# Kernel tuning notes

Measured on AMD Instinct MI355X. Metric: run time of the kernel, lower is better.

## Reference

```python
import jax, jax.numpy as jnp
import numpy as np

B, N, X, Y, W1, W2 = 2, 6, 8, 8, 8, 8
DIM, HEADS, DHEAD = 128, 4, 32
HD = HEADS * DHEAD
EPS = 1e-5


def setup_inputs() -> dict:
    key = jax.random.key(0)
    ks = jax.random.split(key, 12)
    d = {}
    d['q'] = jax.random.normal(ks[0], (B, N, X, Y, W1, W2, DIM), jnp.float32)
    d['k'] = jax.random.normal(ks[1], (B, N, X, Y, W1, W2, DIM), jnp.float32)
    d['v'] = jax.random.normal(ks[2], (B, N, X, Y, W1, W2, DIM), jnp.float32)
    d['skip'] = jax.random.normal(ks[3], (B, X, Y, W1, W2, DIM), jnp.float32)
    d['head_gate'] = jax.random.uniform(ks[4], (HEADS,), jnp.float32, 0.5, 1.5)
    # LayerNorm affine params (slightly perturbed so grads are nontrivial)
    d['ln_q_w'] = 1.0 + 0.1 * jax.random.normal(ks[5], (DIM,), jnp.float32)
    d['ln_q_b'] = jnp.zeros((DIM,), jnp.float32)
    d['ln_k_w'] = 1.0 + 0.1 * jax.random.normal(ks[6], (DIM,), jnp.float32)
    d['ln_k_b'] = jnp.zeros((DIM,), jnp.float32)
    d['ln_v_w'] = 1.0 + 0.1 * jax.random.normal(ks[7], (DIM,), jnp.float32)
    d['ln_v_b'] = jnp.zeros((DIM,), jnp.float32)
    # Linear weights, stored as (in, out) so x @ w + b
    s = 0.02
    d['wq'] = s * jax.random.normal(ks[8], (DIM, HD), jnp.float32)
    d['bq'] = jnp.zeros((HD,), jnp.float32)
    d['wk'] = s * jax.random.normal(ks[9], (DIM, HD), jnp.float32)
    d['bk'] = jnp.zeros((HD,), jnp.float32)
    d['wv'] = s * jax.random.normal(ks[10], (DIM, HD), jnp.float32)
    d['bv'] = jnp.zeros((HD,), jnp.float32)
    d['wp'] = s * jax.random.normal(ks[11], (HD, DIM), jnp.float32)
    d['bp'] = jnp.zeros((DIM,), jnp.float32)
    return d


def _ln(x, w, b):
    mu = jnp.mean(x, axis=-1, keepdims=True)
    var = jnp.mean(jnp.square(x - mu), axis=-1, keepdims=True)
    return (x - mu) * jax.lax.rsqrt(var + EPS) * w + b


def _windows(t):
    # (b, n, x, y, w1, w2, d) -> (b, x*y, n*w1*w2, d)
    b, n, x, y, w1, w2, dd = t.shape
    return t.transpose(0, 2, 3, 1, 4, 5, 6).reshape(b, x * y, n * w1 * w2, dd)


def _heads(t):
    # (b, l, t, HEADS*DHEAD) -> (b, m, l, t, DHEAD)
    b, l, tt, _ = t.shape
    return t.reshape(b, l, tt, HEADS, DHEAD).transpose(0, 3, 1, 2, 4)


def reference(q, k, v, skip, head_gate,
              ln_q_w, ln_q_b, ln_k_w, ln_k_b, ln_v_w, ln_v_b,
              wq, bq, wk, bk, wv, bv, wp, bp):
    b, n, x, y, w1, w2, _ = q.shape
    scale = DHEAD ** -0.5
    qh = _heads(_ln(_windows(q), ln_q_w, ln_q_b) @ wq + bq) * scale
    kh = _heads(_ln(_windows(k), ln_k_w, ln_k_b) @ wk + bk)
    vh = _heads(_ln(_windows(v), ln_v_w, ln_v_b) @ wv + bv)
    # per-window attention: l = x*y windows, Q = K = n*w1*w2 tokens
    dot = jnp.einsum('bmlqd,bmlkd->bmlqk', qh, kh)
    dot = dot * head_gate[None, :, None, None, None]
    att = jax.nn.softmax(dot, axis=-1)
    a = jnp.einsum('bmlqk,bmlkd->bmlqd', att, vh)
    a = a.transpose(0, 2, 3, 1, 4).reshape(b, x * y, n * w1 * w2, HD)
    out = a.reshape(b, x, y, n, w1, w2, HD).transpose(0, 3, 1, 2, 4, 5, 6)
    z = out @ wp + bp          # (b, n, x, y, w1, w2, dim)
    z = jnp.mean(z, axis=1)    # mean over agents n
    return z + skip
```

## Files before the change

kernel.cpp:

```cpp
#include <hip/hip_runtime.h>
#include <hip/hip_bf16.h>
#include <cstddef>

#define NB     2
#define NA     6
#define NWIN   64
#define NTOK   384
#define DIM    128
#define NHEADS 4
#define DHEAD  32

typedef __attribute__((ext_vector_type(8))) short short8;
typedef __attribute__((ext_vector_type(4))) float f32x4;

__device__ __forceinline__ unsigned short f2bf(float f) {
    __hip_bfloat16 h = __float2bfloat16(f);
    return *reinterpret_cast<unsigned short*>(&h);
}
__device__ __forceinline__ float bf2f(unsigned short u) {
    union { unsigned int i; float f; } x; x.i = ((unsigned int)u) << 16; return x.f;
}

#define QSCALE (0.17677669529663687f * 1.4426950408889634f)

__global__ __launch_bounds__(256) void wprep_kernel(
    const float* __restrict__ wq, const float* __restrict__ wk,
    const float* __restrict__ wv,
    const float* __restrict__ lnqw, const float* __restrict__ lnkw,
    const float* __restrict__ lnvw,
    const float* __restrict__ lnqb, const float* __restrict__ lnkb,
    const float* __restrict__ lnvb,
    const float* __restrict__ bq, const float* __restrict__ bk,
    const float* __restrict__ bv, const float* __restrict__ gate,
    unsigned short* __restrict__ wt,
    float* __restrict__ scol, float* __restrict__ tcol)
{
    const int bid = blockIdx.x;
    if (bid < 192) {
        const int e = bid * 256 + threadIdx.x;
        const int mat = e >> 14, i = e & 16383;
        const int kk = i >> 7, c = i & 127;
        const float* src = (mat == 0) ? wq : (mat == 1) ? wk : wv;
        const float* lnw = (mat == 0) ? lnqw : (mat == 1) ? lnkw : lnvw;
        const float s = (mat == 0) ? (QSCALE * gate[c >> 5]) : 1.0f;
        wt[(mat << 14) + c * DIM + kk] = f2bf(src[i] * lnw[kk] * s);
        return;
    }
    const int mat = bid - 192;
    const int c = threadIdx.x;
    if (c >= DIM) return;
    const float* src  = (mat == 0) ? wq : (mat == 1) ? wk : wv;
    const float* lnw  = (mat == 0) ? lnqw : (mat == 1) ? lnkw : lnvw;
    const float* lnb  = (mat == 0) ? lnqb : (mat == 1) ? lnkb : lnvb;
    const float* bias = (mat == 0) ? bq : (mat == 1) ? bk : bv;
    float sa[8] = {0.f,0.f,0.f,0.f,0.f,0.f,0.f,0.f};
    float ta[8] = {0.f,0.f,0.f,0.f,0.f,0.f,0.f,0.f};
#pragma unroll
    for (int k0 = 0; k0 < DIM; k0 += 8) {
        float w0 = src[(k0+0)*DIM+c], w1 = src[(k0+1)*DIM+c];
        float w2 = src[(k0+2)*DIM+c], w3 = src[(k0+3)*DIM+c];
        float w4 = src[(k0+4)*DIM+c], w5 = src[(k0+5)*DIM+c];
        float w6 = src[(k0+6)*DIM+c], w7 = src[(k0+7)*DIM+c];
        sa[0] += lnw[k0+0]*w0; ta[0] += lnb[k0+0]*w0;
        sa[1] += lnw[k0+1]*w1; ta[1] += lnb[k0+1]*w1;
        sa[2] += lnw[k0+2]*w2; ta[2] += lnb[k0+2]*w2;
        sa[3] += lnw[k0+3]*w3; ta[3] += lnb[k0+3]*w3;
        sa[4] += lnw[k0+4]*w4; ta[4] += lnb[k0+4]*w4;
        sa[5] += lnw[k0+5]*w5; ta[5] += lnb[k0+5]*w5;
        sa[6] += lnw[k0+6]*w6; ta[6] += lnb[k0+6]*w6;
        sa[7] += lnw[k0+7]*w7; ta[7] += lnb[k0+7]*w7;
    }
    const float s = ((sa[0]+sa[1])+(sa[2]+sa[3]))+((sa[4]+sa[5])+(sa[6]+sa[7]));
    const float t = ((ta[0]+ta[1])+(ta[2]+ta[3]))+((ta[4]+ta[5])+(ta[6]+ta[7]));
    const float qs = (mat == 0) ? (QSCALE * gate[c >> 5]) : 1.0f;
    scol[mat * DIM + c] = s * qs;
    tcol[mat * DIM + c] = (t + bias[c]) * qs;
}

#define ACC8(p, q) do { \
    s  += ((p.x + p.y) + (p.z + p.w)) + ((q.x + q.y) + (q.z + q.w)); \
    s2 += ((p.x*p.x + p.y*p.y) + (p.z*p.z + p.w*p.w)) \
        + ((q.x*q.x + q.y*q.y) + (q.z*q.z + q.w*q.w)); } while (0)
#define CVT8(p, q) ({ short8 o_; \
    o_[0]=(short)f2bf(p.x); o_[1]=(short)f2bf(p.y); o_[2]=(short)f2bf(p.z); o_[3]=(short)f2bf(p.w); \
    o_[4]=(short)f2bf(q.x); o_[5]=(short)f2bf(q.y); o_[6]=(short)f2bf(q.z); o_[7]=(short)f2bf(q.w); o_; })

__global__ __launch_bounds__(384) void proj_kernel(
    const float* __restrict__ qx, const float* __restrict__ kx,
    const float* __restrict__ vx,
    const unsigned short* __restrict__ wt,
    const float* __restrict__ scol, const float* __restrict__ tcol,
    unsigned short* __restrict__ qh, unsigned short* __restrict__ kh,
    unsigned short* __restrict__ vh)
{
    __shared__ unsigned short Wl[DIM * DIM];

    const int bid  = blockIdx.x;
    const int mode = bid >> 8;
    const int rr   = bid & 255;
    const int b = rr >> 7, l = (rr >> 1) & 63, ng = rr & 1;

    const float* xin = (mode == 0) ? qx : (mode == 1) ? kx : vx;
    const unsigned short* wtm = wt + (mode << 14);
    const float* sc = scol + mode * DIM;
    const float* tc = tcol + mode * DIM;
    unsigned short* outp = (mode == 0) ? qh : (mode == 1) ? kh : vh;

    const int wv_ = threadIdx.x / 64;
    const int lane = threadIdx.x & 63;
    const int g = lane >> 4, qc = lane & 15;
    const int n  = ng * 3 + (wv_ >> 1);
    const int t0 = (wv_ & 1) * 32;

    short8 wbuf0 = {0,0,0,0,0,0,0,0}, wbuf1 = wbuf0, wbuf2 = wbuf0,
           wbuf3 = wbuf0, wbuf4 = wbuf0, wbuf5 = wbuf0;
    {
        const int e0 = threadIdx.x;
        wbuf0 = *(const short8*)&wtm[(e0 +    0) * 8];
        wbuf1 = *(const short8*)&wtm[(e0 +  384) * 8];
        wbuf2 = *(const short8*)&wtm[(e0 +  768) * 8];
        wbuf3 = *(const short8*)&wtm[(e0 + 1152) * 8];
        wbuf4 = *(const short8*)&wtm[(e0 + 1536) * 8];
        if (e0 + 1920 < 2048) wbuf5 = *(const short8*)&wtm[(e0 + 1920) * 8];
    }

    const float* xp0 = xin + ((size_t)((b * NA + n) * NWIN + l) * 64 + t0 + qc) * DIM + 8 * g;
    const float* xp1 = xp0 + 16 * DIM;
    const float4 u0 = *(const float4*)(xp0 + 0);
    const float4 u1 = *(const float4*)(xp0 + 4);
    const float4 u2 = *(const float4*)(xp0 + 32);
    const float4 u3 = *(const float4*)(xp0 + 36);
    const float4 u4 = *(const float4*)(xp0 + 64);
    const float4 u5 = *(const float4*)(xp0 + 68);
    const float4 u6 = *(const float4*)(xp0 + 96);
    const float4 u7 = *(const float4*)(xp0 + 100);
    const float4 y0 = *(const float4*)(xp1 + 0);
    const float4 y1 = *(const float4*)(xp1 + 4);
    const float4 y2 = *(const float4*)(xp1 + 32);
    const float4 y3 = *(const float4*)(xp1 + 36);
    const float4 y4 = *(const float4*)(xp1 + 64);
    const float4 y5 = *(const float4*)(xp1 + 68);
    const float4 y6 = *(const float4*)(xp1 + 96);
    const float4 y7 = *(const float4*)(xp1 + 100);

    {
        const int e0 = threadIdx.x;
#define WSTORE(eo, bufv) do { const int e_ = e0 + eo; \
        const int col_ = e_ >> 4, k8_ = (e_ & 15) * 8; \
        *(short8*)&Wl[col_ * DIM + (k8_ ^ ((col_ & 7) << 3))] = bufv; } while (0)
        WSTORE(0, wbuf0); WSTORE(384, wbuf1); WSTORE(768, wbuf2);
        WSTORE(1152, wbuf3); WSTORE(1536, wbuf4);
        if (e0 + 1920 < 2048) WSTORE(1920, wbuf5);
#undef WSTORE
    }

    float mu0, rs0, mu1, rs1;
    {
        float s = 0.f, s2 = 0.f;
        ACC8(u0, u1); ACC8(u2, u3); ACC8(u4, u5); ACC8(u6, u7);
        s  += __shfl_xor(s, 16);  s  += __shfl_xor(s, 32);
        s2 += __shfl_xor(s2, 16); s2 += __shfl_xor(s2, 32);
        mu0 = s * (1.0f / 128.0f);
        rs0 = rsqrtf(s2 * (1.0f / 128.0f) - mu0 * mu0 + 1e-5f);
    }
    {
        float s = 0.f, s2 = 0.f;
        ACC8(y0, y1); ACC8(y2, y3); ACC8(y4, y5); ACC8(y6, y7);
        s  += __shfl_xor(s, 16);  s  += __shfl_xor(s, 32);
        s2 += __shfl_xor(s2, 16); s2 += __shfl_xor(s2, 32);
        mu1 = s * (1.0f / 128.0f);
        rs1 = rsqrtf(s2 * (1.0f / 128.0f) - mu1 * mu1 + 1e-5f);
    }

    short8 af0[4], af1[4];
    af0[0] = CVT8(u0, u1); af0[1] = CVT8(u2, u3);
    af0[2] = CVT8(u4, u5); af0[3] = CVT8(u6, u7);
    af1[0] = CVT8(y0, y1); af1[1] = CVT8(y2, y3);
    af1[2] = CVT8(y4, y5); af1[3] = CVT8(y6, y7);
    __syncthreads();

    float m0[4], r0[4], m1[4], r1[4];
    if (mode == 2) {
#pragma unroll
        for (int r = 0; r < 4; ++r) {
            m0[r] = __shfl(mu0, 4 * g + r); r0[r] = __shfl(rs0, 4 * g + r);
            m1[r] = __shfl(mu1, 4 * g + r); r1[r] = __shfl(rs1, 4 * g + r);
        }
    }

    const f32x4 z = {0.f, 0.f, 0.f, 0.f};
    const int swz = (qc & 7) << 3;

#pragma unroll
    for (int ct = 0; ct < 8; ++ct) {
        const int col = ct * 16 + qc;
        short8 wf[4];
#pragma unroll
        for (int c = 0; c < 4; ++c)
            wf[c] = *(const short8*)&Wl[col * DIM + ((c * 32 + 8 * g) ^ swz)];

        f32x4 a0 = z, a1 = z;
        if (mode == 2) {
#pragma unroll
            for (int c = 0; c < 4; ++c) {
                a0 = __builtin_amdgcn_mfma_f32_16x16x32_bf16(af0[c], wf[c], a0, 0, 0, 0);
                a1 = __builtin_amdgcn_mfma_f32_16x16x32_bf16(af1[c], wf[c], a1, 0, 0, 0);
            }
            const float s_c = sc[col], t_c = tc[col];
            const int head = ct >> 1;
            const int d = (ct & 1) * 16 + qc;
            const size_t rowb = ((size_t)(b * NHEADS + head) * NWIN + l) * DHEAD + d;
            unsigned short* dst = outp + rowb * NTOK + n * 64 + t0 + 4 * g;
            ushort4 o;
            o.x = f2bf(r0[0] * (a0[0] - m0[0] * s_c) + t_c);
            o.y = f2bf(r0[1] * (a0[1] - m0[1] * s_c) + t_c);
            o.z = f2bf(r0[2] * (a0[2] - m0[2] * s_c) + t_c);
            o.w = f2bf(r0[3] * (a0[3] - m0[3] * s_c) + t_c);
            *(ushort4*)&dst[0] = o;
            o.x = f2bf(r1[0] * (a1[0] - m1[0] * s_c) + t_c);
            o.y = f2bf(r1[1] * (a1[1] - m1[1] * s_c) + t_c);
            o.z = f2bf(r1[2] * (a1[2] - m1[2] * s_c) + t_c);
            o.w = f2bf(r1[3] * (a1[3] - m1[3] * s_c) + t_c);
            *(ushort4*)&dst[16] = o;
        } else {
#pragma unroll
            for (int c = 0; c < 4; ++c) {
                a0 = __builtin_amdgcn_mfma_f32_16x16x32_bf16(wf[c], af0[c], a0, 0, 0, 0);
                a1 = __builtin_amdgcn_mfma_f32_16x16x32_bf16(wf[c], af1[c], a1, 0, 0, 0);
            }
            const int head = ct >> 1;
            const int d0 = (ct & 1) * 16 + 4 * g;
            const float4 s4 = *(const float4*)&sc[ct * 16 + 4 * g];
            const float4 t4 = *(const float4*)&tc[ct * 16 + 4 * g];
            const size_t hb = (size_t)(b * NHEADS + head) * NWIN + l;
            unsigned short* dst = outp + (hb * NTOK + n * 64 + t0 + qc) * DHEAD + d0;
            ushort4 o;
            o.x = f2bf(rs0 * (a0[0] - mu0 * s4.x) + t4.x);
            o.y = f2bf(rs0 * (a0[1] - mu0 * s4.y) + t4.y);
            o.z = f2bf(rs0 * (a0[2] - mu0 * s4.z) + t4.z);
            o.w = f2bf(rs0 * (a0[3] - mu0 * s4.w) + t4.w);
            *(ushort4*)&dst[0] = o;
            o.x = f2bf(rs1 * (a1[0] - mu1 * s4.x) + t4.x);
            o.y = f2bf(rs1 * (a1[1] - mu1 * s4.y) + t4.y);
            o.z = f2bf(rs1 * (a1[2] - mu1 * s4.z) + t4.z);
            o.w = f2bf(rs1 * (a1[3] - mu1 * s4.w) + t4.w);
            *(ushort4*)&dst[16 * DHEAD] = o;
        }
    }
}

__global__ __launch_bounds__(256) void attn_kernel(
    const unsigned short* __restrict__ qh, const unsigned short* __restrict__ kh,
    const unsigned short* __restrict__ vt, unsigned short* __restrict__ aout)
{
    __shared__ unsigned short P[4][3][16][40];

    const int tid  = threadIdx.x;
    const int w    = tid >> 6;
    const int lane = tid & 63;
    const int g    = lane >> 4;
    const int qc   = lane & 15;

    const int raw = blockIdx.x;
    const int p    = (raw >> 4) * 8 + (raw & 7);
    const int half = (raw >> 3) & 1;
    const int b = p >> 8, h = (p >> 6) & 3, l = p & 63;
    const size_t base = (size_t)((b * NHEADS + h) * NWIN + l) * (NTOK * DHEAD);
    const unsigned short* Qp = qh + base;
    const unsigned short* Kp = kh + base;
    const unsigned short* Vp = vt + base;

    short8 qf[3];
#pragma unroll
    for (int j = 0; j < 3; ++j)
        qf[j] = *(const short8*)(Qp + (size_t)(((half * 4 + w) * 3 + j) * 16 + qc) * DHEAD + 8 * g);

    f32x4 o0[3], o1[3];
    float psum[3];
    const f32x4 z = {0.f, 0.f, 0.f, 0.f};
#pragma unroll
    for (int j = 0; j < 3; ++j) { o0[j] = z; o1[j] = z; psum[j] = 0.f; }

    for (int kc = 0; kc < 12; ++kc) {
        const int k0 = kc * 32;
        const short8 ka0 = *(const short8*)(Kp + (size_t)(k0 + qc) * DHEAD + 8 * g);
        const short8 ka1 = *(const short8*)(Kp + (size_t)(k0 + 16 + qc) * DHEAD + 8 * g);
        const short8 vb0 = *(const short8*)(Vp + (size_t)qc * NTOK + k0 + 8 * g);
        const short8 vb1 = *(const short8*)(Vp + (size_t)(16 + qc) * NTOK + k0 + 8 * g);

#pragma unroll
        for (int j = 0; j < 3; ++j) {
            f32x4 s0 = __builtin_amdgcn_mfma_f32_16x16x32_bf16(ka0, qf[j], z, 0, 0, 0);
            f32x4 s1 = __builtin_amdgcn_mfma_f32_16x16x32_bf16(ka1, qf[j], z, 0, 0, 0);
            const float e0 = exp2f(s0[0]), e1 = exp2f(s0[1]), e2 = exp2f(s0[2]), e3 = exp2f(s0[3]);
            const float e4 = exp2f(s1[0]), e5 = exp2f(s1[1]), e6 = exp2f(s1[2]), e7 = exp2f(s1[3]);
            psum[j] += ((e0 + e1) + (e2 + e3)) + ((e4 + e5) + (e6 + e7));
            ushort4 pw0, pw1;
            pw0.x = f2bf(e0); pw0.y = f2bf(e1); pw0.z = f2bf(e2); pw0.w = f2bf(e3);
            pw1.x = f2bf(e4); pw1.y = f2bf(e5); pw1.z = f2bf(e6); pw1.w = f2bf(e7);
            *(ushort4*)&P[w][j][qc][4 * g]      = pw0;
            *(ushort4*)&P[w][j][qc][16 + 4 * g] = pw1;
        }
#pragma unroll
        for (int j = 0; j < 3; ++j) {
            const short8 pa = *(const short8*)&P[w][j][qc][8 * g];
            o0[j] = __builtin_amdgcn_mfma_f32_16x16x32_bf16(pa, vb0, o0[j], 0, 0, 0);
            o1[j] = __builtin_amdgcn_mfma_f32_16x16x32_bf16(pa, vb1, o1[j], 0, 0, 0);
        }
    }

#pragma unroll
    for (int j = 0; j < 3; ++j) {
        float ps = psum[j];
        ps += __shfl_xor(ps, 16);
        ps += __shfl_xor(ps, 32);
        const float inv = 1.0f / ps;
        const int q0 = ((half * 4 + w) * 3 + j) * 16;
        const size_t ob = ((size_t)(b * NWIN + l) * NTOK + q0) * (NHEADS * DHEAD) + h * DHEAD + qc;
#pragma unroll
        for (int r = 0; r < 4; ++r) {
            const float iv = __shfl(inv, 4 * g + r);
            aout[ob + (size_t)(4 * g + r) * (NHEADS * DHEAD)]      = f2bf(o0[j][r] * iv);
            aout[ob + (size_t)(4 * g + r) * (NHEADS * DHEAD) + 16] = f2bf(o1[j][r] * iv);
        }
    }
}

__global__ __launch_bounds__(256) void outproj_kernel(
    const unsigned short* __restrict__ a, const float* __restrict__ wp,
    const float* __restrict__ bp, const float* __restrict__ skip,
    float* __restrict__ outp)
{
    __shared__ float at[DIM * 68];
    __shared__ float wl[DIM * 64];

    const int tid = threadIdx.x;
    const int bid = blockIdx.x;
    const int b = bid >> 7, l = (bid >> 1) & 63, cg = bid & 1;
    const int c0 = cg * 64;

#pragma unroll
    for (int rep = 0; rep < 8; ++rep) {
        const int idx = rep * 256 + tid;
        const int row = idx >> 4, cc4 = idx & 15;
        *(float4*)&wl[row * 64 + cc4 * 4] = *(const float4*)&wp[row * 128 + c0 + cc4 * 4];
    }

    const size_t abase = (size_t)(b * NWIN + l) * NTOK * DIM;
#pragma unroll
    for (int r = 0; r < 32; ++r) {
        const int f = tid + 256 * r;
        const int w_ = f >> 7, d = f & 127;
        float s = 0.f;
#pragma unroll
        for (int n = 0; n < NA; ++n)
            s += bf2f(a[abase + (size_t)(n * 64 + w_) * DIM + d]);
        at[d * 68 + w_] = s * (1.0f / 6.0f);
    }
    __syncthreads();

    const int cx = tid & 15, ty = tid >> 4;
    float acc[4][4];
#pragma unroll
    for (int i = 0; i < 4; ++i)
#pragma unroll
        for (int j = 0; j < 4; ++j) acc[i][j] = 0.f;

#pragma unroll 4
    for (int i = 0; i < DIM; ++i) {
        const float4 wa = *(const float4*)&wl[i * 64 + 4 * cx];
        const float4 aa = *(const float4*)&at[i * 68 + 4 * ty];
        acc[0][0] += aa.x * wa.x; acc[0][1] += aa.x * wa.y; acc[0][2] += aa.x * wa.z; acc[0][3] += aa.x * wa.w;
        acc[1][0] += aa.y * wa.x; acc[1][1] += aa.y * wa.y; acc[1][2] += aa.y * wa.z; acc[1][3] += aa.y * wa.w;
        acc[2][0] += aa.z * wa.x; acc[2][1] += aa.z * wa.y; acc[2][2] += aa.z * wa.z; acc[2][3] += aa.z * wa.w;
        acc[3][0] += aa.w * wa.x; acc[3][1] += aa.w * wa.y; acc[3][2] += aa.w * wa.z; acc[3][3] += aa.w * wa.w;
    }

    const float4 bb = *(const float4*)&bp[c0 + 4 * cx];
#pragma unroll
    for (int u = 0; u < 4; ++u) {
        const int w_ = 4 * ty + u;
        const size_t oidx = ((size_t)(b * NWIN + l) * 64 + w_) * DIM + c0 + 4 * cx;
        const float4 sk = *(const float4*)&skip[oidx];
        float4 o;
        o.x = acc[u][0] + bb.x + sk.x;
        o.y = acc[u][1] + bb.y + sk.y;
        o.z = acc[u][2] + bb.z + sk.z;
        o.w = acc[u][3] + bb.w + sk.w;
        *(float4*)&outp[oidx] = o;
    }
}

extern "C" void kernel_launch(void* const* d_in, const int* in_sizes, int n_in,
                              void* d_out, int out_size, void* d_ws, size_t ws_size,
                              hipStream_t stream) {
    const float* q      = (const float*)d_in[0];
    const float* k      = (const float*)d_in[1];
    const float* v      = (const float*)d_in[2];
    const float* skip   = (const float*)d_in[3];
    const float* gate   = (const float*)d_in[4];
    const float* ln_q_w = (const float*)d_in[5];
    const float* ln_q_b = (const float*)d_in[6];
    const float* ln_k_w = (const float*)d_in[7];
    const float* ln_k_b = (const float*)d_in[8];
    const float* ln_v_w = (const float*)d_in[9];
    const float* ln_v_b = (const float*)d_in[10];
    const float* wq     = (const float*)d_in[11];
    const float* bq     = (const float*)d_in[12];
    const float* wk     = (const float*)d_in[13];
    const float* bk     = (const float*)d_in[14];
    const float* wv     = (const float*)d_in[15];
    const float* bv     = (const float*)d_in[16];
    const float* wp     = (const float*)d_in[17];
    const float* bp     = (const float*)d_in[18];
    float* outp = (float*)d_out;

    const size_t per = (size_t)NB * NHEADS * NWIN * NTOK * DHEAD;
    unsigned short* qh = (unsigned short*)d_ws;
    unsigned short* kh = qh + per;
    unsigned short* vh = kh + per;
    unsigned short* wt = vh + per;
    unsigned short* a  = wt + 3 * 16384;
    float* scol = (float*)(a + per);
    float* tcol = scol + 3 * DIM;

    wprep_kernel<<<195, 256, 0, stream>>>(wq, wk, wv, ln_q_w, ln_k_w, ln_v_w,
                                          ln_q_b, ln_k_b, ln_v_b, bq, bk, bv,
                                          gate, wt, scol, tcol);
    proj_kernel<<<768, 384, 0, stream>>>(q, k, v, wt, scol, tcol, qh, kh, vh);
    attn_kernel<<<NB * NHEADS * NWIN * 2, 256, 0, stream>>>(qh, kh, vh, a);
    outproj_kernel<<<NB * NWIN * 2, 256, 0, stream>>>(a, wp, bp, skip, outp);
}
```

Baseline: 75.52 us.

## Fuse LayerNorm+QKV projection into per-head attention kernel with LDS-resident K/V

```diff
diff --git a/kernel.cpp b/kernel.cpp
--- a/kernel.cpp
+++ b/kernel.cpp
@@ -19,6 +19,9 @@
 }
 __device__ __forceinline__ float bf2f(unsigned short u) {
     union { unsigned int i; float f; } x; x.i = ((unsigned int)u) << 16; return x.f;
+}
+__device__ __forceinline__ unsigned int pk2(float a, float b) {
+    return (unsigned int)f2bf(a) | ((unsigned int)f2bf(b) << 16);
 }
 
 #define QSCALE (0.17677669529663687f * 1.4426950408889634f)
@@ -85,243 +88,251 @@
     o_[0]=(short)f2bf(p.x); o_[1]=(short)f2bf(p.y); o_[2]=(short)f2bf(p.z); o_[3]=(short)f2bf(p.w); \
     o_[4]=(short)f2bf(q.x); o_[5]=(short)f2bf(q.y); o_[6]=(short)f2bf(q.z); o_[7]=(short)f2bf(q.w); o_; })
 
-__global__ __launch_bounds__(384) void proj_kernel(
+__device__ __forceinline__ void ln_unit(
+    const float* __restrict__ xp, float& mu, float& rs, short8* __restrict__ af)
+{
+    const float4 u0 = *(const float4*)(xp + 0);
+    const float4 u1 = *(const float4*)(xp + 4);
+    const float4 u2 = *(const float4*)(xp + 32);
+    const float4 u3 = *(const float4*)(xp + 36);
+    const float4 u4 = *(const float4*)(xp + 64);
+    const float4 u5 = *(const float4*)(xp + 68);
+    const float4 u6 = *(const float4*)(xp + 96);
+    const float4 u7 = *(const float4*)(xp + 100);
+    float s = 0.f, s2 = 0.f;
+    ACC8(u0, u1); ACC8(u2, u3); ACC8(u4, u5); ACC8(u6, u7);
+    s  += __shfl_xor(s, 16);  s  += __shfl_xor(s, 32);
+    s2 += __shfl_xor(s2, 16); s2 += __shfl_xor(s2, 32);
+    mu = s * (1.0f / 128.0f);
+    rs = rsqrtf(s2 * (1.0f / 128.0f) - mu * mu + 1e-5f);
+    af[0] = CVT8(u0, u1); af[1] = CVT8(u2, u3);
+    af[2] = CVT8(u4, u5); af[3] = CVT8(u6, u7);
+}
+
+__global__ __launch_bounds__(384) void fattn_kernel(
     const float* __restrict__ qx, const float* __restrict__ kx,
     const float* __restrict__ vx,
     const unsigned short* __restrict__ wt,
     const float* __restrict__ scol, const float* __restrict__ tcol,
-    unsigned short* __restrict__ qh, unsigned short* __restrict__ kh,
-    unsigned short* __restrict__ vh)
+    unsigned short* __restrict__ aout)
 {
-    __shared__ unsigned short Wl[DIM * DIM];
-
-    const int bid  = blockIdx.x;
-    const int mode = bid >> 8;
-    const int rr   = bid & 255;
-    const int b = rr >> 7, l = (rr >> 1) & 63, ng = rr & 1;
-
-    const float* xin = (mode == 0) ? qx : (mode == 1) ? kx : vx;
-    const unsigned short* wtm = wt + (mode << 14);
-    const float* sc = scol + mode * DIM;
-    const float* tc = tcol + mode * DIM;
-    unsigned short* outp = (mode == 0) ? qh : (mode == 1) ? kh : vh;
+    __shared__ unsigned short Wl[3 * 32 * DIM];
+    __shared__ unsigned short Kl[NTOK * 32];
+    __shared__ unsigned short Vl[32 * 392];
+
+    const int id = blockIdx.x;
+    const int r_ = id & 7, rest = id >> 3;
+    const int h = rest & 3, gq = rest >> 2;
+    const int group = gq * 8 + r_;
+    const int b = group >> 6, l = group & 63;
 
     const int wv_ = threadIdx.x / 64;
     const int lane = threadIdx.x & 63;
     const int g = lane >> 4, qc = lane & 15;
-    const int n  = ng * 3 + (wv_ >> 1);
-    const int t0 = (wv_ & 1) * 32;
-
-    short8 wbuf0 = {0,0,0,0,0,0,0,0}, wbuf1 = wbuf0, wbuf2 = wbuf0,
-           wbuf3 = wbuf0, wbuf4 = wbuf0, wbuf5 = wbuf0;
+    const int swz = (qc & 7) << 3;
+
     {
-        const int e0 = threadIdx.x;
-        wbuf0 = *(const short8*)&wtm[(e0 +    0) * 8];
-        wbuf1 = *(const short8*)&wtm[(e0 +  384) * 8];
-        wbuf2 = *(const short8*)&wtm[(e0 +  768) * 8];
-        wbuf3 = *(const short8*)&wtm[(e0 + 1152) * 8];
-        wbuf4 = *(const short8*)&wtm[(e0 + 1536) * 8];
-        if (e0 + 1920 < 2048) wbuf5 = *(const short8*)&wtm[(e0 + 1920) * 8];
-    }
-
-    const float* xp0 = xin + ((size_t)((b * NA + n) * NWIN + l) * 64 + t0 + qc) * DIM + 8 * g;
-    const float* xp1 = xp0 + 16 * DIM;
-    const float4 u0 = *(const float4*)(xp0 + 0);
-    const float4 u1 = *(const float4*)(xp0 + 4);
-    const float4 u2 = *(const float4*)(xp0 + 32);
-    const float4 u3 = *(const float4*)(xp0 + 36);
-    const float4 u4 = *(const float4*)(xp0 + 64);
-    const float4 u5 = *(const float4*)(xp0 + 68);
-    const float4 u6 = *(const float4*)(xp0 + 96);
-    const float4 u7 = *(const float4*)(xp0 + 100);
-    const float4 y0 = *(const float4*)(xp1 + 0);
-    const float4 y1 = *(const float4*)(xp1 + 4);
-    const float4 y2 = *(const float4*)(xp1 + 32);
-    const float4 y3 = *(const float4*)(xp1 + 36);
-    const float4 y4 = *(const float4*)(xp1 + 64);
-    const float4 y5 = *(const float4*)(xp1 + 68);
-    const float4 y6 = *(const float4*)(xp1 + 96);
-    const float4 y7 = *(const float4*)(xp1 + 100);
-
-    {
-        const int e0 = threadIdx.x;
-#define WSTORE(eo, bufv) do { const int e_ = e0 + eo; \
-        const int col_ = e_ >> 4, k8_ = (e_ & 15) * 8; \
-        *(short8*)&Wl[col_ * DIM + (k8_ ^ ((col_ & 7) << 3))] = bufv; } while (0)
-        WSTORE(0, wbuf0); WSTORE(384, wbuf1); WSTORE(768, wbuf2);
-        WSTORE(1152, wbuf3); WSTORE(1536, wbuf4);
-        if (e0 + 1920 < 2048) WSTORE(1920, wbuf5);
-#undef WSTORE
-    }
-
-    float mu0, rs0, mu1, rs1;
-    {
-        float s = 0.f, s2 = 0.f;
-        ACC8(u0, u1); ACC8(u2, u3); ACC8(u4, u5); ACC8(u6, u7);
-        s  += __shfl_xor(s, 16);  s  += __shfl_xor(s, 32);
-        s2 += __shfl_xor(s2, 16); s2 += __shfl_xor(s2, 32);
-        mu0 = s * (1.0f / 128.0f);
-        rs0 = rsqrtf(s2 * (1.0f / 128.0f) - mu0 * mu0 + 1e-5f);
-    }
-    {
-        float s = 0.f, s2 = 0.f;
-        ACC8(y0, y1); ACC8(y2, y3); ACC8(y4, y5); ACC8(y6, y7);
-        s  += __shfl_xor(s, 16);  s  += __shfl_xor(s, 32);
-        s2 += __shfl_xor(s2, 16); s2 += __shfl_xor(s2, 32);
-        mu1 = s * (1.0f / 128.0f);
-        rs1 = rsqrtf(s2 * (1.0f / 128.0f) - mu1 * mu1 + 1e-5f);
-    }
-
-    short8 af0[4], af1[4];
-    af0[0] = CVT8(u0, u1); af0[1] = CVT8(u2, u3);
-    af0[2] = CVT8(u4, u5); af0[3] = CVT8(u6, u7);
-    af1[0] = CVT8(y0, y1); af1[1] = CVT8(y2, y3);
-    af1[2] = CVT8(y4, y5); af1[3] = CVT8(y6, y7);
+        const int t0 = threadIdx.x;
+        const int c0 = t0, c1 = t0 + 384, c2 = t0 + 768, c3 = t0 + 1152;
+#define WSRC(c) (wt + ((c) >> 9) * 16384 + (h * 32 + (((c) & 511) >> 4)) * DIM + ((c) & 15) * 8)
+        const short8 wb0 = *(const short8*)WSRC(c0);
+        const short8 wb1 = *(const short8*)WSRC(c1);
+        const short8 wb2 = *(const short8*)WSRC(c2);
+        const short8 wb3 = *(const short8*)WSRC(c3);
+#undef WSRC
+#define WDST(c, v) { const int m_ = (c) >> 9, rem_ = (c) & 511; \
+        const int col_ = rem_ >> 4, jj_ = rem_ & 15; \
+        *(short8*)&Wl[m_ * 4096 + col_ * DIM + ((jj_ ^ (col_ & 7)) * 8)] = v; }
+        WDST(c0, wb0); WDST(c1, wb1); WDST(c2, wb2); WDST(c3, wb3);
+#undef WDST
+    }
     __syncthreads();
 
-    float m0[4], r0[4], m1[4], r1[4];
-    if (mode == 2) {
-#pragma unroll
-        for (int r = 0; r < 4; ++r) {
-            m0[r] = __shfl(mu0, 4 * g + r); r0[r] = __shfl(rs0, 4 * g + r);
-            m1[r] = __shfl(mu1, 4 * g + r); r1[r] = __shfl(rs1, 4 * g + r);
-        }
-    }
-
     const f32x4 z = {0.f, 0.f, 0.f, 0.f};
-    const int swz = (qc & 7) << 3;
-
-#pragma unroll
-    for (int ct = 0; ct < 8; ++ct) {
-        const int col = ct * 16 + qc;
-        short8 wf[4];
-#pragma unroll
-        for (int c = 0; c < 4; ++c)
-            wf[c] = *(const short8*)&Wl[col * DIM + ((c * 32 + 8 * g) ^ swz)];
-
-        f32x4 a0 = z, a1 = z;
-        if (mode == 2) {
-#pragma unroll
-            for (int c = 0; c < 4; ++c) {
-                a0 = __builtin_amdgcn_mfma_f32_16x16x32_bf16(af0[c], wf[c], a0, 0, 0, 0);
-                a1 = __builtin_amdgcn_mfma_f32_16x16x32_bf16(af1[c], wf[c], a1, 0, 0, 0);
-            }
-            const float s_c = sc[col], t_c = tc[col];
-            const int head = ct >> 1;
-            const int d = (ct & 1) * 16 + qc;
-            const size_t rowb = ((size_t)(b * NHEADS + head) * NWIN + l) * DHEAD + d;
-            unsigned short* dst = outp + rowb * NTOK + n * 64 + t0 + 4 * g;
-            ushort4 o;
-            o.x = f2bf(r0[0] * (a0[0] - m0[0] * s_c) + t_c);
-            o.y = f2bf(r0[1] * (a0[1] - m0[1] * s_c) + t_c);
-            o.z = f2bf(r0[2] * (a0[2] - m0[2] * s_c) + t_c);
-            o.w = f2bf(r0[3] * (a0[3] - m0[3] * s_c) + t_c);
-            *(ushort4*)&dst[0] = o;
-            o.x = f2bf(r1[0] * (a1[0] - m1[0] * s_c) + t_c);
-            o.y = f2bf(r1[1] * (a1[1] - m1[1] * s_c) + t_c);
-            o.z = f2bf(r1[2] * (a1[2] - m1[2] * s_c) + t_c);
-            o.w = f2bf(r1[3] * (a1[3] - m1[3] * s_c) + t_c);
-            *(ushort4*)&dst[16] = o;
-        } else {
-#pragma unroll
-            for (int c = 0; c < 4; ++c) {
-                a0 = __builtin_amdgcn_mfma_f32_16x16x32_bf16(wf[c], af0[c], a0, 0, 0, 0);
-                a1 = __builtin_amdgcn_mfma_f32_16x16x32_bf16(wf[c], af1[c], a1, 0, 0, 0);
-            }
-            const int head = ct >> 1;
-            const int d0 = (ct & 1) * 16 + 4 * g;
-            const float4 s4 = *(const float4*)&sc[ct * 16 + 4 * g];
-            const float4 t4 = *(const float4*)&tc[ct * 16 + 4 * g];
-            const size_t hb = (size_t)(b * NHEADS + head) * NWIN + l;
-            unsigned short* dst = outp + (hb * NTOK + n * 64 + t0 + qc) * DHEAD + d0;
-            ushort4 o;
-            o.x = f2bf(rs0 * (a0[0] - mu0 * s4.x) + t4.x);
-            o.y = f2bf(rs0 * (a0[1] - mu0 * s4.y) + t4.y);
-            o.z = f2bf(rs0 * (a0[2] - mu0 * s4.z) + t4.z);
-            o.w = f2bf(rs0 * (a0[3] - mu0 * s4.w) + t4.w);
-            *(ushort4*)&dst[0] = o;
-            o.x = f2bf(rs1 * (a1[0] - mu1 * s4.x) + t4.x);
-            o.y = f2bf(rs1 * (a1[1] - mu1 * s4.y) + t4.y);
-            o.z = f2bf(rs1 * (a1[2] - mu1 * s4.z) + t4.z);
-            o.w = f2bf(rs1 * (a1[3] - mu1 * s4.w) + t4.w);
-            *(ushort4*)&dst[16 * DHEAD] = o;
-        }
-    }
-}
-
-__global__ __launch_bounds__(256) void attn_kernel(
-    const unsigned short* __restrict__ qh, const unsigned short* __restrict__ kh,
-    const unsigned short* __restrict__ vt, unsigned short* __restrict__ aout)
-{
-    __shared__ unsigned short P[4][3][16][40];
-
-    const int tid  = threadIdx.x;
-    const int w    = tid >> 6;
-    const int lane = tid & 63;
-    const int g    = lane >> 4;
-    const int qc   = lane & 15;
-
-    const int raw = blockIdx.x;
-    const int p    = (raw >> 4) * 8 + (raw & 7);
-    const int half = (raw >> 3) & 1;
-    const int b = p >> 8, h = (p >> 6) & 3, l = p & 63;
-    const size_t base = (size_t)((b * NHEADS + h) * NWIN + l) * (NTOK * DHEAD);
-    const unsigned short* Qp = qh + base;
-    const unsigned short* Kp = kh + base;
-    const unsigned short* Vp = vt + base;
-
-    short8 qf[3];
-#pragma unroll
-    for (int j = 0; j < 3; ++j)
-        qf[j] = *(const short8*)(Qp + (size_t)(((half * 4 + w) * 3 + j) * 16 + qc) * DHEAD + 8 * g);
-
-    f32x4 o0[3], o1[3];
-    float psum[3];
-    const f32x4 z = {0.f, 0.f, 0.f, 0.f};
-#pragma unroll
-    for (int j = 0; j < 3; ++j) { o0[j] = z; o1[j] = z; psum[j] = 0.f; }
-
-    for (int kc = 0; kc < 12; ++kc) {
-        const int k0 = kc * 32;
-        const short8 ka0 = *(const short8*)(Kp + (size_t)(k0 + qc) * DHEAD + 8 * g);
-        const short8 ka1 = *(const short8*)(Kp + (size_t)(k0 + 16 + qc) * DHEAD + 8 * g);
-        const short8 vb0 = *(const short8*)(Vp + (size_t)qc * NTOK + k0 + 8 * g);
-        const short8 vb1 = *(const short8*)(Vp + (size_t)(16 + qc) * NTOK + k0 + 8 * g);
-
-#pragma unroll
-        for (int j = 0; j < 3; ++j) {
-            f32x4 s0 = __builtin_amdgcn_mfma_f32_16x16x32_bf16(ka0, qf[j], z, 0, 0, 0);
-            f32x4 s1 = __builtin_amdgcn_mfma_f32_16x16x32_bf16(ka1, qf[j], z, 0, 0, 0);
-            const float e0 = exp2f(s0[0]), e1 = exp2f(s0[1]), e2 = exp2f(s0[2]), e3 = exp2f(s0[3]);
-            const float e4 = exp2f(s1[0]), e5 = exp2f(s1[1]), e6 = exp2f(s1[2]), e7 = exp2f(s1[3]);
-            psum[j] += ((e0 + e1) + (e2 + e3)) + ((e4 + e5) + (e6 + e7));
-            ushort4 pw0, pw1;
-            pw0.x = f2bf(e0); pw0.y = f2bf(e1); pw0.z = f2bf(e2); pw0.w = f2bf(e3);
-            pw1.x = f2bf(e4); pw1.y = f2bf(e5); pw1.z = f2bf(e6); pw1.w = f2bf(e7);
-            *(ushort4*)&P[w][j][qc][4 * g]      = pw0;
-            *(ushort4*)&P[w][j][qc][16 + 4 * g] = pw1;
-        }
-#pragma unroll
-        for (int j = 0; j < 3; ++j) {
-            const short8 pa = *(const short8*)&P[w][j][qc][8 * g];
-            o0[j] = __builtin_amdgcn_mfma_f32_16x16x32_bf16(pa, vb0, o0[j], 0, 0, 0);
-            o1[j] = __builtin_amdgcn_mfma_f32_16x16x32_bf16(pa, vb1, o1[j], 0, 0, 0);
-        }
-    }
-
-#pragma unroll
-    for (int j = 0; j < 3; ++j) {
-        float ps = psum[j];
-        ps += __shfl_xor(ps, 16);
-        ps += __shfl_xor(ps, 32);
-        const float inv = 1.0f / ps;
-        const int q0 = ((half * 4 + w) * 3 + j) * 16;
-        const size_t ob = ((size_t)(b * NWIN + l) * NTOK + q0) * (NHEADS * DHEAD) + h * DHEAD + qc;
-#pragma unroll
-        for (int r = 0; r < 4; ++r) {
-            const float iv = __shfl(inv, 4 * g + r);
-            aout[ob + (size_t)(4 * g + r) * (NHEADS * DHEAD)]      = f2bf(o0[j][r] * iv);
-            aout[ob + (size_t)(4 * g + r) * (NHEADS * DHEAD) + 16] = f2bf(o1[j][r] * iv);
+    uint2 qd[4][2];
+
+#pragma unroll
+    for (int j = 0; j < 4; ++j) {
+        const int u = 4 * wv_ + j;
+        const int n = u >> 2;
+        const int tloc = 16 * u;
+        const size_t xoff = (((size_t)(b * NA + n) * NWIN + l) * 64 + (u & 3) * 16 + qc) * DIM + 8 * g;
+
+        {
+            float mu, rs; short8 af[4];
+            ln_unit(qx + xoff, mu, rs, af);
+#pragma unroll
+            for (int ct = 0; ct < 2; ++ct) {
+                const int lc = ct * 16 + qc;
+                f32x4 acc = z;
+#pragma unroll
+                for (int c = 0; c < 4; ++c) {
+                    const short8 wf = *(const short8*)&Wl[lc * DIM + ((c * 32 + 8 * g) ^ swz)];
+                    acc = __builtin_amdgcn_mfma_f32_16x16x32_bf16(wf, af[c], acc, 0, 0, 0);
+                }
+                const float4 s4 = *(const float4*)&scol[h * 32 + ct * 16 + 4 * g];
+                const float4 t4 = *(const float4*)&tcol[h * 32 + ct * 16 + 4 * g];
+                qd[j][ct].x = pk2(rs * (acc[0] - mu * s4.x) + t4.x,
+                                  rs * (acc[1] - mu * s4.y) + t4.y);
+                qd[j][ct].y = pk2(rs * (acc[2] - mu * s4.z) + t4.z,
+                                  rs * (acc[3] - mu * s4.w) + t4.w);
+            }
+        }
+        {
+            float mu, rs; short8 af[4];
+            ln_unit(kx + xoff, mu, rs, af);
+#pragma unroll
+            for (int ct = 0; ct < 2; ++ct) {
+                const int lc = ct * 16 + qc;
+                f32x4 acc = z;
+#pragma unroll
+                for (int c = 0; c < 4; ++c) {
+                    const short8 wf = *(const short8*)&Wl[4096 + lc * DIM + ((c * 32 + 8 * g) ^ swz)];
+                    acc = __builtin_amdgcn_mfma_f32_16x16x32_bf16(wf, af[c], acc, 0, 0, 0);
+                }
+                const float4 s4 = *(const float4*)&scol[DIM + h * 32 + ct * 16 + 4 * g];
+                const float4 t4 = *(const float4*)&tcol[DIM + h * 32 + ct * 16 + 4 * g];
+                ushort4 o;
+                o.x = f2bf(rs * (acc[0] - mu * s4.x) + t4.x);
+                o.y = f2bf(rs * (acc[1] - mu * s4.y) + t4.y);
+                o.z = f2bf(rs * (acc[2] - mu * s4.z) + t4.z);
+                o.w = f2bf(rs * (acc[3] - mu * s4.w) + t4.w);
+                *(ushort4*)&Kl[(tloc + qc) * 32 + ct * 16 + 4 * g] = o;
+            }
+        }
+        {
+            float mu, rs; short8 af[4];
+            ln_unit(vx + xoff, mu, rs, af);
+            float m4[4], r4[4];
+#pragma unroll
+            for (int r = 0; r < 4; ++r) {
+                m4[r] = __shfl(mu, 4 * g + r);
+                r4[r] = __shfl(rs, 4 * g + r);
+            }
+#pragma unroll
+            for (int ct = 0; ct < 2; ++ct) {
+                const int lc = ct * 16 + qc;
+                f32x4 acc = z;
+#pragma unroll
+                for (int c = 0; c < 4; ++c) {
+                    const short8 wf = *(const short8*)&Wl[8192 + lc * DIM + ((c * 32 + 8 * g) ^ swz)];
+                    acc = __builtin_amdgcn_mfma_f32_16x16x32_bf16(af[c], wf, acc, 0, 0, 0);
+                }
+                const float s_c = scol[2 * DIM + h * 32 + lc];
+                const float t_c = tcol[2 * DIM + h * 32 + lc];
+                ushort4 o;
+                o.x = f2bf(r4[0] * (acc[0] - m4[0] * s_c) + t_c);
+                o.y = f2bf(r4[1] * (acc[1] - m4[1] * s_c) + t_c);
+                o.z = f2bf(r4[2] * (acc[2] - m4[2] * s_c) + t_c);
+                o.w = f2bf(r4[3] * (acc[3] - m4[3] * s_c) + t_c);
+                *(ushort4*)&Vl[lc * 392 + tloc + 4 * g] = o;
+            }
+        }
+    }
+    __syncthreads();
+
+    const int srcA = (((2 * g) & 3) << 4) + qc;
+    const int srcB = (((2 * g + 1) & 3) << 4) + qc;
+    const bool lo = (g < 2);
+
+#pragma unroll
+    for (int jp = 0; jp < 2; ++jp) {
+        short8 qfA, qfB;
+        {
+            const int d0 = qd[2 * jp][0].x, d1 = qd[2 * jp][0].y;
+            const int d2 = qd[2 * jp][1].x, d3 = qd[2 * jp][1].y;
+            const int a0 = __shfl(d0, srcA), a1 = __shfl(d1, srcA);
+            const int a2 = __shfl(d2, srcA), a3 = __shfl(d3, srcA);
+            const int b0 = __shfl(d0, srcB), b1 = __shfl(d1, srcB);
+            const int b2 = __shfl(d2, srcB), b3 = __shfl(d3, srcB);
+            int4 t; t.x = lo ? a0 : a2; t.y = lo ? a1 : a3;
+            t.z = lo ? b0 : b2; t.w = lo ? b1 : b3;
+            qfA = *(short8*)&t;
+        }
+        {
+            const int d0 = qd[2 * jp + 1][0].x, d1 = qd[2 * jp + 1][0].y;
+            const int d2 = qd[2 * jp + 1][1].x, d3 = qd[2 * jp + 1][1].y;
+            const int a0 = __shfl(d0, srcA), a1 = __shfl(d1, srcA);
+            const int a2 = __shfl(d2, srcA), a3 = __shfl(d3, srcA);
+            const int b0 = __shfl(d0, srcB), b1 = __shfl(d1, srcB);
+            const int b2 = __shfl(d2, srcB), b3 = __shfl(d3, srcB);
+            int4 t; t.x = lo ? a0 : a2; t.y = lo ? a1 : a3;
+            t.z = lo ? b0 : b2; t.w = lo ? b1 : b3;
+            qfB = *(short8*)&t;
+        }
+
+        f32x4 oA0 = z, oA1 = z, oB0 = z, oB1 = z;
+        float psA = 0.f, psB = 0.f;
+
+        for (int kc = 0; kc < 12; ++kc) {
+            const int k0 = kc * 32;
+            const short8 ka0 = *(const short8*)&Kl[(k0 + qc) * 32 + 8 * g];
+            const short8 ka1 = *(const short8*)&Kl[(k0 + 16 + qc) * 32 + 8 * g];
+            const short8 vb0 = *(const short8*)&Vl[qc * 392 + k0 + 8 * g];
+            const short8 vb1 = *(const short8*)&Vl[(16 + qc) * 392 + k0 + 8 * g];
+            {
+                f32x4 s0 = __builtin_amdgcn_mfma_f32_16x16x32_bf16(ka0, qfA, z, 0, 0, 0);
+                f32x4 s1 = __builtin_amdgcn_mfma_f32_16x16x32_bf16(ka1, qfA, z, 0, 0, 0);
+                const float e0 = exp2f(s0[0]), e1 = exp2f(s0[1]), e2 = exp2f(s0[2]), e3 = exp2f(s0[3]);
+                const float e4 = exp2f(s1[0]), e5 = exp2f(s1[1]), e6 = exp2f(s1[2]), e7 = exp2f(s1[3]);
+                psA += ((e0 + e1) + (e2 + e3)) + ((e4 + e5) + (e6 + e7));
+                const int d0 = pk2(e0, e1), d1 = pk2(e2, e3);
+                const int d2 = pk2(e4, e5), d3 = pk2(e6, e7);
+                const int a0 = __shfl(d0, srcA), a1 = __shfl(d1, srcA);
+                const int a2 = __shfl(d2, srcA), a3 = __shfl(d3, srcA);
+                const int b0 = __shfl(d0, srcB), b1 = __shfl(d1, srcB);
+                const int b2 = __shfl(d2, srcB), b3 = __shfl(d3, srcB);
+                int4 t; t.x = lo ? a0 : a2; t.y = lo ? a1 : a3;
+                t.z = lo ? b0 : b2; t.w = lo ? b1 : b3;
+                const short8 pa = *(short8*)&t;
+                oA0 = __builtin_amdgcn_mfma_f32_16x16x32_bf16(pa, vb0, oA0, 0, 0, 0);
+                oA1 = __builtin_amdgcn_mfma_f32_16x16x32_bf16(pa, vb1, oA1, 0, 0, 0);
+            }
+            {
+                f32x4 s0 = __builtin_amdgcn_mfma_f32_16x16x32_bf16(ka0, qfB, z, 0, 0, 0);
+                f32x4 s1 = __builtin_amdgcn_mfma_f32_16x16x32_bf16(ka1, qfB, z, 0, 0, 0);
+                const float e0 = exp2f(s0[0]), e1 = exp2f(s0[1]), e2 = exp2f(s0[2]), e3 = exp2f(s0[3]);
+                const float e4 = exp2f(s1[0]), e5 = exp2f(s1[1]), e6 = exp2f(s1[2]), e7 = exp2f(s1[3]);
+                psB += ((e0 + e1) + (e2 + e3)) + ((e4 + e5) + (e6 + e7));
+                const int d0 = pk2(e0, e1), d1 = pk2(e2, e3);
+                const int d2 = pk2(e4, e5), d3 = pk2(e6, e7);
+                const int a0 = __shfl(d0, srcA), a1 = __shfl(d1, srcA);
+                const int a2 = __shfl(d2, srcA), a3 = __shfl(d3, srcA);
+                const int b0 = __shfl(d0, srcB), b1 = __shfl(d1, srcB);
+                const int b2 = __shfl(d2, srcB), b3 = __shfl(d3, srcB);
+                int4 t; t.x = lo ? a0 : a2; t.y = lo ? a1 : a3;
+                t.z = lo ? b0 : b2; t.w = lo ? b1 : b3;
+                const short8 pa = *(short8*)&t;
+                oB0 = __builtin_amdgcn_mfma_f32_16x16x32_bf16(pa, vb0, oB0, 0, 0, 0);
+                oB1 = __builtin_amdgcn_mfma_f32_16x16x32_bf16(pa, vb1, oB1, 0, 0, 0);
+            }
+        }
+
+        {
+            float ps = psA;
+            ps += __shfl_xor(ps, 16); ps += __shfl_xor(ps, 32);
+            const float inv = 1.0f / ps;
+            const int q0 = 64 * wv_ + 16 * (2 * jp);
+            const size_t ob = ((size_t)(b * NWIN + l) * NTOK + q0) * (NHEADS * DHEAD) + h * DHEAD + qc;
+#pragma unroll
+            for (int r = 0; r < 4; ++r) {
+                const float iv = __shfl(inv, 4 * g + r);
+                aout[ob + (size_t)(4 * g + r) * (NHEADS * DHEAD)]      = f2bf(oA0[r] * iv);
+                aout[ob + (size_t)(4 * g + r) * (NHEADS * DHEAD) + 16] = f2bf(oA1[r] * iv);
+            }
+        }
+        {
+            float ps = psB;
+            ps += __shfl_xor(ps, 16); ps += __shfl_xor(ps, 32);
+            const float inv = 1.0f / ps;
+            const int q0 = 64 * wv_ + 16 * (2 * jp + 1);
+            const size_t ob = ((size_t)(b * NWIN + l) * NTOK + q0) * (NHEADS * DHEAD) + h * DHEAD + qc;
+#pragma unroll
+            for (int r = 0; r < 4; ++r) {
+                const float iv = __shfl(inv, 4 * g + r);
+                aout[ob + (size_t)(4 * g + r) * (NHEADS * DHEAD)]      = f2bf(oB0[r] * iv);
+                aout[ob + (size_t)(4 * g + r) * (NHEADS * DHEAD) + 16] = f2bf(oB1[r] * iv);
+            }
         }
     }
 }
@@ -415,11 +426,8 @@
     const float* bp     = (const float*)d_in[18];
     float* outp = (float*)d_out;
 
-    const size_t per = (size_t)NB * NHEADS * NWIN * NTOK * DHEAD;
-    unsigned short* qh = (unsigned short*)d_ws;
-    unsigned short* kh = qh + per;
-    unsigned short* vh = kh + per;
-    unsigned short* wt = vh + per;
+    const size_t per = (size_t)NB * NWIN * NTOK * DIM;
+    unsigned short* wt = (unsigned short*)d_ws;
     unsigned short* a  = wt + 3 * 16384;
     float* scol = (float*)(a + per);
     float* tcol = scol + 3 * DIM;
@@ -427,7 +435,6 @@
     wprep_kernel<<<195, 256, 0, stream>>>(wq, wk, wv, ln_q_w, ln_k_w, ln_v_w,
                                           ln_q_b, ln_k_b, ln_v_b, bq, bk, bv,
                                           gate, wt, scol, tcol);
-    proj_kernel<<<768, 384, 0, stream>>>(q, k, v, wt, scol, tcol, qh, kh, vh);
-    attn_kernel<<<NB * NHEADS * NWIN * 2, 256, 0, stream>>>(qh, kh, vh, a);
+    fattn_kernel<<<NB * NHEADS * NWIN, 384, 0, stream>>>(q, k, v, wt, scol, tcol, a);
     outproj_kernel<<<NB * NWIN * 2, 256, 0, stream>>>(a, wp, bp, skip, outp);
 }
```

Result: slower. 102.5 us (+35.7%).
